# Optimization experiments

Measured on AMD Instinct MI355X. Metric: run time of the kernel, lower is better.

Reference implementation:

```python
import jax, jax.numpy as jnp
import numpy as np
import math

NUM_IMGS, BATCH, DIM, H, W = 2, 32, 512, 18, 18
NUM_POS = 2
KEY_DIM = 128
NUM_LAYERS = 6
TEMP = 30.0
NORM_EPS = 1e-5
L2_EPS = 1e-12
NORM_SCALE = math.sqrt(1.0 / (DIM * 4 * 4))


def setup_inputs() -> dict:
    key = jax.random.key(0)
    ks = jax.random.split(key, 8)
    L_mem = NUM_POS * H * W
    return {
        "tgt": jax.random.normal(ks[0], (NUM_IMGS, BATCH, DIM, H, W), jnp.float32),
        "pos_embed": jax.random.normal(ks[1], (NUM_IMGS, BATCH, DIM, H, W), jnp.float32),
        "memory": jax.random.normal(ks[2], (L_mem, BATCH, DIM), jnp.float32),
        "pos": jax.random.uniform(ks[3], (NUM_POS, BATCH, H, W), jnp.float32),
        "Wk_self": jax.random.normal(ks[4], (KEY_DIM, DIM), jnp.float32) * 0.02,
        "bk_self": jnp.zeros((KEY_DIM,), jnp.float32),
        "Wk_cross": jax.random.normal(ks[5], (KEY_DIM, DIM), jnp.float32) * 0.02,
        "bk_cross": jnp.zeros((KEY_DIM,), jnp.float32),
    }


def _l2norm(x):
    n = jnp.sqrt(jnp.sum(x * x, axis=-1, keepdims=True))
    return x / jnp.maximum(n, L2_EPS)


def _attn(q, k, v, Wk, bk):
    # q:[Lq,B,D] k:[Lk,B,D] v:[Lk,B,D]; custom RelationUnit attention
    wq = _l2norm(q @ Wk.T + bk)              # [Lq,B,K]
    wk = _l2norm(k @ Wk.T + bk)              # [Lk,B,K]
    scores = jnp.einsum('qbk,sbk->bqs', wq, wk) * TEMP
    aff = jax.nn.softmax(scores, axis=-1)    # [B,Lq,Lk]
    return jnp.einsum('bqs,sbd->qbd', aff, v)


def _inorm(src):
    # src:[n*h*w, B, D]; InstanceL2Norm over (D,H,W) per (img,batch)
    x = src.reshape(NUM_IMGS, H * W, BATCH, DIM)
    ss = jnp.sum(x * x, axis=(1, 3), keepdims=True)
    x = x * (NORM_SCALE * jnp.sqrt((DIM * H * W) / (ss + NORM_EPS)))
    return x.reshape(NUM_IMGS * H * W, BATCH, DIM)


def reference(tgt, pos_embed, memory, pos, Wk_self, bk_self, Wk_cross, bk_cross):
    n, b, d, h, w = tgt.shape
    # flatten to [n*h*w, B, D]
    def flat(x):
        return x.reshape(n, b, d, h * w).transpose(0, 3, 1, 2).reshape(-1, b, d)
    x = flat(tgt)
    pe = flat(pos_embed)
    # pos: [num_pos,B,h,w] -> [num_pos*h*w, B, D] (value broadcast across D)
    num_pos = pos.shape[0]
    p = pos.reshape(num_pos, b, 1, h * w).transpose(0, 3, 1, 2).reshape(-1, b, 1)
    p = jnp.broadcast_to(p, (p.shape[0], b, d))
    mem_p = memory * p

    for _ in range(NUM_LAYERS):  # all layers share weights (_get_clones has no deepcopy)
        x = x + pe * 0.001
        x = _inorm(x + _attn(x, x, x, Wk_self, bk_self))
        mask = _attn(x, memory, p, Wk_cross, bk_cross)
        t2 = _inorm(x * mask)
        t3 = _attn(x, memory, mem_p, Wk_cross, bk_cross)
        t4 = _inorm(x + t3)
        x = _inorm(t2 + t4)

    out_feat = x.reshape(n, h, w, b, d).transpose(0, 3, 4, 1, 2).reshape(-1, d, h, w)
    return (x, out_feat)
```

## Files before the change

kernel.cpp:

```cpp
#include <hip/hip_runtime.h>
#include <math.h>

#define NI  2
#define BB  32
#define DD  512
#define HWX 324
#define LL  648
#define MM  648
#define KX  128

#define TEMPF  30.0f
#define NEPSF  1e-5f
#define L2EPSF 1e-12f
#define DHWF   165888.0f
#define NSDF   0.011048543456039806f

typedef float f8v __attribute__((ext_vector_type(8)));

__global__ void k_flat(const float* __restrict__ src, const float* __restrict__ pe,
                       float* __restrict__ x) {
  size_t idx = (size_t)blockIdx.x * 256 + threadIdx.x;
  int r = (int)(idx >> 9), d = (int)(idx & 511);
  int l = r >> 5, b = r & 31;
  int i = l / HWX, s = l % HWX;
  size_t sidx = ((size_t)(i * BB + b) * DD + d) * HWX + s;
  float v = src[sidx];
  float t = __fmul_rn(pe[sidx], 0.001f);
  x[idx] = __fadd_rn(v, t);
}

__global__ void k_pos(const float* __restrict__ pos, float* __restrict__ ps) {
  int idx = blockIdx.x * 256 + threadIdx.x;
  int l = idx >> 5, b = idx & 31;
  int j = l / HWX, s = l % HWX;
  ps[idx] = pos[((size_t)(j * BB + b)) * HWX + s];
}

__global__ void k_memp(const float* __restrict__ mem, const float* __restrict__ ps,
                       float* __restrict__ memp) {
  size_t idx = (size_t)blockIdx.x * 256 + threadIdx.x;
  memp[idx] = __fmul_rn(mem[idx], ps[idx >> 9]);
}

__global__ void k_wt(const float* __restrict__ W, float* __restrict__ Wt) {
  int idx = blockIdx.x * 256 + threadIdx.x;
  int k = idx & 127, d = idx >> 7;
  Wt[idx] = W[(size_t)k * DD + d];
}

__global__ __launch_bounds__(512) void k_projt(const float* __restrict__ A,
                                               const float* __restrict__ Wt,
                                               const float* __restrict__ bias,
                                               float* __restrict__ outp) {
  int r0 = blockIdx.x * 128;
  int tid = threadIdx.x, tx = tid & 15, ty = tid >> 4;
  __shared__ float As[128][36];
  __shared__ float Ws[32][132];
  __shared__ float bsh[128];
  __shared__ float sqb[32][129];
  __shared__ float prb[32][8];
  __shared__ float nshs[32];
  if (tid < 128) bsh[tid] = bias[tid];
  float acc[4][8] = {};
  for (int d0 = 0; d0 < 512; d0 += 32) {
#pragma unroll
    for (int n = 0; n < 2; n++) {
      int fi = tid + 512 * n;
      int rr = fi >> 3, dq = (fi & 7) * 4;
      *(float4*)&As[rr][dq] = *(const float4*)(A + (size_t)(r0 + rr) * 512 + d0 + dq);
    }
#pragma unroll
    for (int n = 0; n < 2; n++) {
      int fi = tid + 512 * n;
      int dd2 = fi >> 5, kq = (fi & 31) * 4;
      *(float4*)&Ws[dd2][kq] = *(const float4*)(Wt + (size_t)(d0 + dd2) * 128 + kq);
    }
    __syncthreads();
#pragma unroll 8
    for (int dd2 = 0; dd2 < 32; dd2++) {
      float a[4], w[8];
#pragma unroll
      for (int i = 0; i < 4; i++) a[i] = As[ty + 32 * i][dd2];
#pragma unroll
      for (int j = 0; j < 8; j++) w[j] = Ws[dd2][tx + 16 * j];
#pragma unroll
      for (int i = 0; i < 4; i++)
#pragma unroll
        for (int j = 0; j < 8; j++) acc[i][j] = fmaf(a[i], w[j], acc[i][j]);
    }
    __syncthreads();
  }
  for (int i = 0; i < 4; i++) {
    float val[8];
#pragma unroll
    for (int j = 0; j < 8; j++) {
      val[j] = __fadd_rn(acc[i][j], bsh[tx + 16 * j]);
      sqb[ty][tx + 16 * j] = __fmul_rn(val[j], val[j]);
    }
    __syncthreads();
    if (tid < 256) {
      int row = tid >> 3, jj = tid & 7;
      float rr = sqb[row][jj];
      for (int blk = 1; blk < 16; blk++) rr += sqb[row][blk * 8 + jj];
      prb[row][jj] = rr;
    }
    __syncthreads();
    if (tid < 32) {
      float* p = prb[tid];
      float ss = ((p[0] + p[1]) + (p[2] + p[3])) + ((p[4] + p[5]) + (p[6] + p[7]));
      nshs[tid] = fmaxf(__fsqrt_rn(ss), L2EPSF);
    }
    __syncthreads();
    float nsh = nshs[ty];
    int r = r0 + ty + 32 * i;
#pragma unroll
    for (int j = 0; j < 8; j++)
      outp[(size_t)r * 128 + tx + 16 * j] = __fdiv_rn(val[j], nsh);
    __syncthreads();
  }
}

__global__ __launch_bounds__(256) void k_scoret(const float* __restrict__ wqp,
                                                const float* __restrict__ wkp,
                                                float* __restrict__ sc) {
  int q0 = blockIdx.x * 96, s0 = blockIdx.y * 96, b = blockIdx.z;
  int tid = threadIdx.x, tx = tid & 15, ty = tid >> 4;
  __shared__ float QsT[32][97];
  __shared__ float Ks[96][36];
  float acc[6][6] = {};
  const float4 f40 = make_float4(0.f, 0.f, 0.f, 0.f);
  for (int k0 = 0; k0 < 128; k0 += 32) {
#pragma unroll
    for (int n = 0; n < 3; n++) {
      int fi = tid + 256 * n;
      int rr = fi >> 3, kq = (fi & 7) * 4;
      int q = q0 + rr;
      float4 v = (q < LL) ? *(const float4*)(wqp + ((size_t)q * 32 + b) * 128 + k0 + kq) : f40;
      QsT[kq + 0][rr] = v.x; QsT[kq + 1][rr] = v.y;
      QsT[kq + 2][rr] = v.z; QsT[kq + 3][rr] = v.w;
      int s = s0 + rr;
      float4 w = (s < MM) ? *(const float4*)(wkp + ((size_t)s * 32 + b) * 128 + k0 + kq) : f40;
      *(float4*)&Ks[rr][kq] = w;
    }
    __syncthreads();
#pragma unroll 8
    for (int kk = 0; kk < 32; kk++) {
      float a[6], w[6];
#pragma unroll
      for (int i = 0; i < 6; i++) a[i] = QsT[kk][ty + 16 * i];
#pragma unroll
      for (int j = 0; j < 6; j++) w[j] = Ks[tx + 16 * j][kk];
#pragma unroll
      for (int i = 0; i < 6; i++)
#pragma unroll
        for (int j = 0; j < 6; j++) acc[i][j] = fmaf(a[i], w[j], acc[i][j]);
    }
    __syncthreads();
  }
#pragma unroll
  for (int i = 0; i < 6; i++) {
    int q = q0 + ty + 16 * i;
    if (q >= LL) continue;
    float* orow = sc + ((size_t)b * LL + q) * MM;
#pragma unroll
    for (int j = 0; j < 6; j++) {
      int s = s0 + tx + 16 * j;
      if (s < MM) orow[s] = __fmul_rn(acc[i][j], TEMPF);
    }
  }
}

__global__ __launch_bounds__(256) void k_sm2(float* __restrict__ sc) {
  int row = blockIdx.x;
  float* p = sc + (size_t)row * MM;
  int t = threadIdx.x;
  __shared__ float red[256];
  __shared__ float es[MM];
  __shared__ float prc[64];
  __shared__ float ssum;
  float v0 = p[t], v1 = p[t + 256];
  bool h2 = t < (MM - 512);
  float v2 = h2 ? p[t + 512] : -3.0e38f;
  red[t] = fmaxf(fmaxf(v0, v1), v2);
  __syncthreads();
  for (int off = 128; off; off >>= 1) {
    if (t < off) red[t] = fmaxf(red[t], red[t + off]);
    __syncthreads();
  }
  float mx = red[0];
  float e0 = (float)exp((double)__fsub_rn(v0, mx));
  float e1 = (float)exp((double)__fsub_rn(v1, mx));
  float e2 = h2 ? (float)exp((double)__fsub_rn(v2, mx)) : 0.0f;
  es[t] = e0; es[t + 256] = e1;
  if (h2) es[t + 512] = e2;
  __syncthreads();
  if (t < 64) {
    int c = t >> 3, jj = t & 7;
    int base = c * 80, n = (c == 7) ? 88 : 80;
    float r = es[base + jj];
    for (int i = 8; i < n; i += 8) r += es[base + i + jj];
    prc[t] = r;
  }
  __syncthreads();
  if (t == 0) {
    float pc[8];
#pragma unroll
    for (int c = 0; c < 8; c++) {
      float* pp = prc + c * 8;
      pc[c] = ((pp[0] + pp[1]) + (pp[2] + pp[3])) + ((pp[4] + pp[5]) + (pp[6] + pp[7]));
    }
    float lsum = (pc[0] + pc[1]) + (pc[2] + pc[3]);
    float rsum = (pc[4] + pc[5]) + (pc[6] + pc[7]);
    ssum = lsum + rsum;
  }
  __syncthreads();
  float s = ssum;
  p[t] = __fdiv_rn(e0, s);
  p[t + 256] = __fdiv_rn(e1, s);
  if (h2) p[t + 512] = __fdiv_rn(e2, s);
}

template <int DO_MASK>
__global__ __launch_bounds__(256) void k_applyg(const float* __restrict__ aff,
                                                const float* __restrict__ V,
                                                const float* __restrict__ ps,
                                                float* __restrict__ outp,
                                                float* __restrict__ msk) {
  int dd = blockIdx.x;
  int xcd = dd & 7, j = dd >> 3;
  int b = xcd * 4 + j / 54;
  int q0 = (j % 54) * 12;
  int tid = threadIdx.x;
  const float* abase = aff + ((size_t)b * LL + q0) * MM;
  const float* vbase = V + (size_t)b * 512 + tid * 2;
  float acc0[12] = {};
  float acc1[12] = {};
  for (int s8 = 0; s8 < 81; s8++) {
    float2 v0 = *(const float2*)(vbase + (size_t)(8 * s8 + 0) * 16384);
    float2 v1 = *(const float2*)(vbase + (size_t)(8 * s8 + 1) * 16384);
    float2 v2 = *(const float2*)(vbase + (size_t)(8 * s8 + 2) * 16384);
    float2 v3 = *(const float2*)(vbase + (size_t)(8 * s8 + 3) * 16384);
    float2 v4 = *(const float2*)(vbase + (size_t)(8 * s8 + 4) * 16384);
    float2 v5 = *(const float2*)(vbase + (size_t)(8 * s8 + 5) * 16384);
    float2 v6 = *(const float2*)(vbase + (size_t)(8 * s8 + 6) * 16384);
    float2 v7 = *(const float2*)(vbase + (size_t)(8 * s8 + 7) * 16384);
#pragma unroll
    for (int qq = 0; qq < 12; qq++) {
      f8v a8 = *(const f8v*)(abase + qq * MM + s8 * 8);
      acc0[qq] = fmaf(a8[0], v0.x, acc0[qq]); acc1[qq] = fmaf(a8[0], v0.y, acc1[qq]);
      acc0[qq] = fmaf(a8[1], v1.x, acc0[qq]); acc1[qq] = fmaf(a8[1], v1.y, acc1[qq]);
      acc0[qq] = fmaf(a8[2], v2.x, acc0[qq]); acc1[qq] = fmaf(a8[2], v2.y, acc1[qq]);
      acc0[qq] = fmaf(a8[3], v3.x, acc0[qq]); acc1[qq] = fmaf(a8[3], v3.y, acc1[qq]);
      acc0[qq] = fmaf(a8[4], v4.x, acc0[qq]); acc1[qq] = fmaf(a8[4], v4.y, acc1[qq]);
      acc0[qq] = fmaf(a8[5], v5.x, acc0[qq]); acc1[qq] = fmaf(a8[5], v5.y, acc1[qq]);
      acc0[qq] = fmaf(a8[6], v6.x, acc0[qq]); acc1[qq] = fmaf(a8[6], v6.y, acc1[qq]);
      acc0[qq] = fmaf(a8[7], v7.x, acc0[qq]); acc1[qq] = fmaf(a8[7], v7.y, acc1[qq]);
    }
  }
#pragma unroll
  for (int qq = 0; qq < 12; qq++) {
    float2 r = make_float2(acc0[qq], acc1[qq]);
    *(float2*)(outp + ((size_t)(q0 + qq) * 32 + b) * 512 + tid * 2) = r;
  }
  if (DO_MASK && tid < 12) {
    const float* arow = abase + tid * MM;
    float a = 0.0f;
    for (int s = 0; s < MM; s++) a = fmaf(arow[s], ps[s * 32 + b], a);
    msk[(q0 + tid) * 32 + b] = a;
  }
}

template <int MODE>
__global__ __launch_bounds__(128) void k_na(const float* __restrict__ x,
                                            const float* __restrict__ ao,
                                            const float* __restrict__ msk,
                                            const float* __restrict__ scu,
                                            const float* __restrict__ scv,
                                            float* __restrict__ tU,
                                            float* __restrict__ tV) {
  int s = blockIdx.x;
  int g = blockIdx.y;
  int i = g >> 5, b = g & 31;
  int l = i * HWX + s;
  size_t base = ((size_t)l * BB + b) * DD;
  int t = threadIdx.x;
  __shared__ float squ[DD];
  __shared__ float sqv[DD];
  __shared__ float pru[32];
  __shared__ float prv[32];
  float mk = 0.f, su = 0.f, sv = 0.f;
  if (MODE >= 2) mk = msk[l * BB + b];
  if (MODE == 3) { su = scu[g]; sv = scv[g]; }
  for (int d = t; d < DD; d += 128) {
    float xx = x[base + d];
    if (MODE == 1) {
      float y = __fadd_rn(xx, ao[base + d]);
      squ[d] = __fmul_rn(y, y);
    } else if (MODE == 2) {
      float u = __fmul_rn(xx, mk);
      float v = __fadd_rn(xx, ao[base + d]);
      squ[d] = __fmul_rn(u, u);
      sqv[d] = __fmul_rn(v, v);
    } else {
      float u = __fmul_rn(xx, mk);
      float v = __fadd_rn(xx, ao[base + d]);
      float t2 = __fmul_rn(u, su);
      float t4 = __fmul_rn(v, sv);
      float w = __fadd_rn(t2, t4);
      squ[d] = __fmul_rn(w, w);
    }
  }
  __syncthreads();
  if (t < 32) {
    int c = t >> 3, jj = t & 7, b0 = c * 128;
    float r = squ[b0 + jj];
    for (int blk = 1; blk < 16; blk++) r += squ[b0 + blk * 8 + jj];
    pru[t] = r;
    if (MODE == 2) {
      float r2 = sqv[b0 + jj];
      for (int blk = 1; blk < 16; blk++) r2 += sqv[b0 + blk * 8 + jj];
      prv[t] = r2;
    }
  }
  __syncthreads();
  if (t == 0) {
    float cc[4];
    for (int c = 0; c < 4; c++)
      cc[c] = ((pru[c * 8] + pru[c * 8 + 1]) + (pru[c * 8 + 2] + pru[c * 8 + 3])) +
              ((pru[c * 8 + 4] + pru[c * 8 + 5]) + (pru[c * 8 + 6] + pru[c * 8 + 7]));
    tU[g * HWX + s] = (cc[0] + cc[1]) + (cc[2] + cc[3]);
    if (MODE == 2) {
      for (int c = 0; c < 4; c++)
        cc[c] = ((prv[c * 8] + prv[c * 8 + 1]) + (prv[c * 8 + 2] + prv[c * 8 + 3])) +
                ((prv[c * 8 + 4] + prv[c * 8 + 5]) + (prv[c * 8 + 6] + prv[c * 8 + 7]));
      tV[g * HWX + s] = (cc[0] + cc[1]) + (cc[2] + cc[3]);
    }
  }
}

__global__ void k_fin1(const float* __restrict__ tU, float* __restrict__ scl) {
  int g = threadIdx.x;
  float ss = 0.0f;
  for (int s4 = 0; s4 < 81; s4++) {
    float4 t = *(const float4*)(tU + g * HWX + s4 * 4);
    ss += t.x; ss += t.y; ss += t.z; ss += t.w;
  }
  scl[g] = __fmul_rn(NSDF, __fsqrt_rn(__fdiv_rn(DHWF, __fadd_rn(ss, NEPSF))));
}

__global__ void k_fin2(const float* __restrict__ tU, const float* __restrict__ tV,
                       float* __restrict__ scu, float* __restrict__ scv) {
  int g = threadIdx.x;
  float su = 0.0f, sv = 0.0f;
  for (int s4 = 0; s4 < 81; s4++) {
    float4 t = *(const float4*)(tU + g * HWX + s4 * 4);
    float4 t2 = *(const float4*)(tV + g * HWX + s4 * 4);
    su += t.x; su += t.y; su += t.z; su += t.w;
    sv += t2.x; sv += t2.y; sv += t2.z; sv += t2.w;
  }
  scu[g] = __fmul_rn(NSDF, __fsqrt_rn(__fdiv_rn(DHWF, __fadd_rn(su, NEPSF))));
  scv[g] = __fmul_rn(NSDF, __fsqrt_rn(__fdiv_rn(DHWF, __fadd_rn(sv, NEPSF))));
}

__global__ void k_a1(float* __restrict__ x, const float* __restrict__ ao,
                     const float* __restrict__ scl) {
  size_t idx = (size_t)blockIdx.x * 256 + threadIdx.x;
  int r = (int)(idx >> 9);
  int l = r >> 5, b = r & 31;
  int g = (l / HWX) * BB + b;
  x[idx] = __fmul_rn(__fadd_rn(x[idx], ao[idx]), scl[g]);
}

template <int ADDPE>
__global__ void k_a2(float* __restrict__ x, const float* __restrict__ ao,
                     const float* __restrict__ msk, const float* __restrict__ scu,
                     const float* __restrict__ scv, const float* __restrict__ scw,
                     const float* __restrict__ pe) {
  size_t idx = (size_t)blockIdx.x * 256 + threadIdx.x;
  int r = (int)(idx >> 9);
  int l = r >> 5, b = r & 31;
  int g = (l / HWX) * BB + b;
  float mk = msk[l * BB + b];
  float xx = x[idx];
  float u = __fmul_rn(xx, mk);
  float v = __fadd_rn(xx, ao[idx]);
  float t2 = __fmul_rn(u, scu[g]);
  float t4 = __fmul_rn(v, scv[g]);
  float w = __fadd_rn(t2, t4);
  float res = __fmul_rn(w, scw[g]);
  if (ADDPE) {
    int d = (int)(idx & 511);
    int i = l / HWX, s = l % HWX;
    float t = __fmul_rn(pe[((size_t)(i * BB + b) * DD + d) * HWX + s], 0.001f);
    res = __fadd_rn(res, t);
  }
  x[idx] = res;
}

__global__ void k_o0(const float* __restrict__ x, float* __restrict__ out) {
  size_t idx = (size_t)blockIdx.x * 256 + threadIdx.x;
  out[idx] = x[idx];
}

__global__ void k_o1(const float* __restrict__ x, float* __restrict__ out1) {
  size_t idx = (size_t)blockIdx.x * 256 + threadIdx.x;
  int s = (int)(idx % HWX);
  int d = (int)((idx / HWX) & 511);
  int ib = (int)(idx / ((size_t)HWX * DD));
  int i = ib >> 5, b = ib & 31;
  int l = i * HWX + s;
  out1[idx] = x[((size_t)l * BB + b) * DD + d];
}

extern "C" void kernel_launch(void* const* d_in, const int* in_sizes, int n_in,
                              void* d_out, int out_size, void* d_ws, size_t ws_size,
                              hipStream_t stream) {
  const float* tgt = (const float*)d_in[0];
  const float* pe  = (const float*)d_in[1];
  const float* mem = (const float*)d_in[2];
  const float* pos = (const float*)d_in[3];
  const float* Wks = (const float*)d_in[4];
  const float* bks = (const float*)d_in[5];
  const float* Wkc = (const float*)d_in[6];
  const float* bkc = (const float*)d_in[7];
  float* out = (float*)d_out;

  if (ws_size < (size_t)203240448) return;
  float* f = (float*)d_ws;
  float* x    = f;
  float* ao   = f + 10616832;
  float* memp = f + 21233664;
  float* wq   = f + 31850496;
  float* wkm  = f + 34504704;
  float* sc   = f + 37158912;
  float* msk  = f + 50595840;
  float* ps   = f + 50616576;
  float* tU   = f + 50637312;
  float* tV   = f + 50658048;
  float* scl  = f + 50678784;
  float* scu  = scl + 64;
  float* scv  = scl + 128;
  float* scw  = scl + 192;
  float* Wst  = f + 50679040;
  float* Wct  = f + 50744576;

  k_wt<<<256, 256, 0, stream>>>(Wks, Wst);
  k_wt<<<256, 256, 0, stream>>>(Wkc, Wct);
  k_flat<<<41472, 256, 0, stream>>>(tgt, pe, x);
  k_pos<<<81, 256, 0, stream>>>(pos, ps);
  k_memp<<<41472, 256, 0, stream>>>(mem, ps, memp);
  k_projt<<<162, 512, 0, stream>>>(mem, Wct, bkc, wkm);

  dim3 scg(7, 7, 32);
  dim3 nag(324, 64);
  for (int l = 0; l < 6; l++) {
    k_projt<<<162, 512, 0, stream>>>(x, Wst, bks, wq);
    k_scoret<<<scg, 256, 0, stream>>>(wq, wq, sc);
    k_sm2<<<20736, 256, 0, stream>>>(sc);
    k_applyg<0><<<1728, 256, 0, stream>>>(sc, x, nullptr, ao, nullptr);
    k_na<1><<<nag, 128, 0, stream>>>(x, ao, nullptr, nullptr, nullptr, tU, nullptr);
    k_fin1<<<1, 64, 0, stream>>>(tU, scl);
    k_a1<<<41472, 256, 0, stream>>>(x, ao, scl);
    k_projt<<<162, 512, 0, stream>>>(x, Wct, bkc, wq);
    k_scoret<<<scg, 256, 0, stream>>>(wq, wkm, sc);
    k_sm2<<<20736, 256, 0, stream>>>(sc);
    k_applyg<1><<<1728, 256, 0, stream>>>(sc, memp, ps, ao, msk);
    k_na<2><<<nag, 128, 0, stream>>>(x, ao, msk, nullptr, nullptr, tU, tV);
    k_fin2<<<1, 64, 0, stream>>>(tU, tV, scu, scv);
    k_na<3><<<nag, 128, 0, stream>>>(x, ao, msk, scu, scv, tU, nullptr);
    k_fin1<<<1, 64, 0, stream>>>(tU, scw);
    if (l < 5)
      k_a2<1><<<41472, 256, 0, stream>>>(x, ao, msk, scu, scv, scw, pe);
    else
      k_a2<0><<<41472, 256, 0, stream>>>(x, ao, msk, scu, scv, scw, nullptr);
  }

  k_o0<<<41472, 256, 0, stream>>>(x, out);
  k_o1<<<41472, 256, 0, stream>>>(x, out + (size_t)LL * BB * DD);
}
```

Before: 5.584 ms.

## Move mask reduction into softmax kernel and halve projection tile rows

The mask dot product (affinity row times pos) is moved from the tail of the apply kernel, where only 12 threads per block ran it serially, into the cross-attention softmax kernel. There one thread per row computes it from shared memory right after normalization, which removes an extra serial read of the affinity rows. Separately, the projection kernel now uses 64-row tiles with 256 threads, doubling the block count to 324 to fill more CUs. The softmax kernel gains a second shared buffer and an extra serial 648-length loop per row on thread 0, which may lengthen that kernel.

```diff
diff --git a/kernel.cpp b/kernel.cpp
--- a/kernel.cpp
+++ b/kernel.cpp
@@ -48,41 +48,41 @@
   Wt[idx] = W[(size_t)k * DD + d];
 }
 
-__global__ __launch_bounds__(512) void k_projt(const float* __restrict__ A,
+__global__ __launch_bounds__(256) void k_projt(const float* __restrict__ A,
                                                const float* __restrict__ Wt,
                                                const float* __restrict__ bias,
                                                float* __restrict__ outp) {
-  int r0 = blockIdx.x * 128;
+  int r0 = blockIdx.x * 64;
   int tid = threadIdx.x, tx = tid & 15, ty = tid >> 4;
-  __shared__ float As[128][36];
+  __shared__ float As[64][36];
   __shared__ float Ws[32][132];
   __shared__ float bsh[128];
-  __shared__ float sqb[32][129];
-  __shared__ float prb[32][8];
-  __shared__ float nshs[32];
+  __shared__ float sqb[16][129];
+  __shared__ float prb[16][8];
+  __shared__ float nshs[16];
   if (tid < 128) bsh[tid] = bias[tid];
   float acc[4][8] = {};
   for (int d0 = 0; d0 < 512; d0 += 32) {
 #pragma unroll
     for (int n = 0; n < 2; n++) {
-      int fi = tid + 512 * n;
+      int fi = tid + 256 * n;
       int rr = fi >> 3, dq = (fi & 7) * 4;
       *(float4*)&As[rr][dq] = *(const float4*)(A + (size_t)(r0 + rr) * 512 + d0 + dq);
     }
 #pragma unroll
-    for (int n = 0; n < 2; n++) {
-      int fi = tid + 512 * n;
-      int dd2 = fi >> 5, kq = (fi & 31) * 4;
-      *(float4*)&Ws[dd2][kq] = *(const float4*)(Wt + (size_t)(d0 + dd2) * 128 + kq);
+    for (int n = 0; n < 4; n++) {
+      int fi = tid + 256 * n;
+      int dd = fi >> 5, kq = (fi & 31) * 4;
+      *(float4*)&Ws[dd][kq] = *(const float4*)(Wt + (size_t)(d0 + dd) * 128 + kq);
     }
     __syncthreads();
 #pragma unroll 8
-    for (int dd2 = 0; dd2 < 32; dd2++) {
+    for (int dd = 0; dd < 32; dd++) {
       float a[4], w[8];
 #pragma unroll
-      for (int i = 0; i < 4; i++) a[i] = As[ty + 32 * i][dd2];
-#pragma unroll
-      for (int j = 0; j < 8; j++) w[j] = Ws[dd2][tx + 16 * j];
+      for (int i = 0; i < 4; i++) a[i] = As[ty + 16 * i][dd];
+#pragma unroll
+      for (int j = 0; j < 8; j++) w[j] = Ws[dd][tx + 16 * j];
 #pragma unroll
       for (int i = 0; i < 4; i++)
 #pragma unroll
@@ -98,21 +98,21 @@
       sqb[ty][tx + 16 * j] = __fmul_rn(val[j], val[j]);
     }
     __syncthreads();
-    if (tid < 256) {
+    if (tid < 128) {
       int row = tid >> 3, jj = tid & 7;
       float rr = sqb[row][jj];
       for (int blk = 1; blk < 16; blk++) rr += sqb[row][blk * 8 + jj];
       prb[row][jj] = rr;
     }
     __syncthreads();
-    if (tid < 32) {
+    if (tid < 16) {
       float* p = prb[tid];
       float ss = ((p[0] + p[1]) + (p[2] + p[3])) + ((p[4] + p[5]) + (p[6] + p[7]));
       nshs[tid] = fmaxf(__fsqrt_rn(ss), L2EPSF);
     }
     __syncthreads();
     float nsh = nshs[ty];
-    int r = r0 + ty + 32 * i;
+    int r = r0 + ty + 16 * i;
 #pragma unroll
     for (int j = 0; j < 8; j++)
       outp[(size_t)r * 128 + tx + 16 * j] = __fdiv_rn(val[j], nsh);
@@ -170,14 +170,22 @@
   }
 }
 
-__global__ __launch_bounds__(256) void k_sm2(float* __restrict__ sc) {
+template <int DO_MASK>
+__global__ __launch_bounds__(256) void k_sm2(float* __restrict__ sc,
+                                             const float* __restrict__ ps,
+                                             float* __restrict__ msk) {
   int row = blockIdx.x;
   float* p = sc + (size_t)row * MM;
   int t = threadIdx.x;
   __shared__ float red[256];
   __shared__ float es[MM];
+  __shared__ float psl[MM];
   __shared__ float prc[64];
   __shared__ float ssum;
+  int b = row / LL, q = row - b * LL;
+  if (DO_MASK) {
+    for (int s = t; s < MM; s += 256) psl[s] = ps[s * 32 + b];
+  }
   float v0 = p[t], v1 = p[t + 256];
   bool h2 = t < (MM - 512);
   float v2 = h2 ? p[t + 512] : -3.0e38f;
@@ -215,17 +223,25 @@
   }
   __syncthreads();
   float s = ssum;
-  p[t] = __fdiv_rn(e0, s);
-  p[t + 256] = __fdiv_rn(e1, s);
-  if (h2) p[t + 512] = __fdiv_rn(e2, s);
-}
-
-template <int DO_MASK>
+  float d0 = __fdiv_rn(e0, s), d1 = __fdiv_rn(e1, s);
+  p[t] = d0; p[t + 256] = d1;
+  float d2 = 0.f;
+  if (h2) { d2 = __fdiv_rn(e2, s); p[t + 512] = d2; }
+  if (DO_MASK) {
+    es[t] = d0; es[t + 256] = d1;
+    if (h2) es[t + 512] = d2;
+    __syncthreads();
+    if (t == 0) {
+      float a = 0.0f;
+      for (int ss2 = 0; ss2 < MM; ss2++) a = fmaf(es[ss2], psl[ss2], a);
+      msk[q * 32 + b] = a;
+    }
+  }
+}
+
 __global__ __launch_bounds__(256) void k_applyg(const float* __restrict__ aff,
                                                 const float* __restrict__ V,
-                                                const float* __restrict__ ps,
-                                                float* __restrict__ outp,
-                                                float* __restrict__ msk) {
+                                                float* __restrict__ outp) {
   int dd = blockIdx.x;
   int xcd = dd & 7, j = dd >> 3;
   int b = xcd * 4 + j / 54;
@@ -261,12 +277,6 @@
   for (int qq = 0; qq < 12; qq++) {
     float2 r = make_float2(acc0[qq], acc1[qq]);
     *(float2*)(outp + ((size_t)(q0 + qq) * 32 + b) * 512 + tid * 2) = r;
-  }
-  if (DO_MASK && tid < 12) {
-    const float* arow = abase + tid * MM;
-    float a = 0.0f;
-    for (int s = 0; s < MM; s++) a = fmaf(arow[s], ps[s * 32 + b], a);
-    msk[(q0 + tid) * 32 + b] = a;
   }
 }
 
@@ -449,22 +459,22 @@
   k_flat<<<41472, 256, 0, stream>>>(tgt, pe, x);
   k_pos<<<81, 256, 0, stream>>>(pos, ps);
   k_memp<<<41472, 256, 0, stream>>>(mem, ps, memp);
-  k_projt<<<162, 512, 0, stream>>>(mem, Wct, bkc, wkm);
+  k_projt<<<324, 256, 0, stream>>>(mem, Wct, bkc, wkm);
 
   dim3 scg(7, 7, 32);
   dim3 nag(324, 64);
   for (int l = 0; l < 6; l++) {
-    k_projt<<<162, 512, 0, stream>>>(x, Wst, bks, wq);
+    k_projt<<<324, 256, 0, stream>>>(x, Wst, bks, wq);
     k_scoret<<<scg, 256, 0, stream>>>(wq, wq, sc);
-    k_sm2<<<20736, 256, 0, stream>>>(sc);
-    k_applyg<0><<<1728, 256, 0, stream>>>(sc, x, nullptr, ao, nullptr);
+    k_sm2<0><<<20736, 256, 0, stream>>>(sc, nullptr, nullptr);
+    k_applyg<<<1728, 256, 0, stream>>>(sc, x, ao);
     k_na<1><<<nag, 128, 0, stream>>>(x, ao, nullptr, nullptr, nullptr, tU, nullptr);
     k_fin1<<<1, 64, 0, stream>>>(tU, scl);
     k_a1<<<41472, 256, 0, stream>>>(x, ao, scl);
-    k_projt<<<162, 512, 0, stream>>>(x, Wct, bkc, wq);
+    k_projt<<<324, 256, 0, stream>>>(x, Wct, bkc, wq);
     k_scoret<<<scg, 256, 0, stream>>>(wq, wkm, sc);
-    k_sm2<<<20736, 256, 0, stream>>>(sc);
-    k_applyg<1><<<1728, 256, 0, stream>>>(sc, memp, ps, ao, msk);
+    k_sm2<1><<<20736, 256, 0, stream>>>(sc, ps, msk);
+    k_applyg<<<1728, 256, 0, stream>>>(sc, memp, ao);
     k_na<2><<<nag, 128, 0, stream>>>(x, ao, msk, nullptr, nullptr, tU, tV);
     k_fin2<<<1, 64, 0, stream>>>(tU, tV, scu, scv);
     k_na<3><<<nag, 128, 0, stream>>>(x, ao, msk, scu, scv, tU, nullptr);
```

New measurement: 5.982 ms. 1.07x slower.
